# Kernel tuning notes

Measured on AMD Instinct MI355X. Metric: run time of the kernel, lower is better.

Reference implementation:

```python
import jax, jax.numpy as jnp
import numpy as np

N_NODES = 100000
N_EDGES = 1600000
N_FEAT = 128
N_HID = 128
N_CLASS = 10
N_GRAPHS = 512
BN_EPS = 1e-5


def setup_inputs() -> dict:
    key = jax.random.key(0)
    ks = jax.random.split(key, 12)
    x = jax.random.normal(ks[0], (N_NODES, N_FEAT), dtype=jnp.float32)
    edge_index = jax.random.randint(ks[1], (2, N_EDGES), 0, N_NODES, dtype=jnp.int32)
    batch = jnp.sort(jax.random.randint(ks[2], (N_NODES,), 0, N_GRAPHS, dtype=jnp.int32))
    s1 = 1.0 / np.sqrt(N_FEAT)
    s2 = 1.0 / np.sqrt(N_HID)
    W1 = jax.random.uniform(ks[3], (N_FEAT, N_HID), jnp.float32, -s1, s1)
    b1 = jax.random.uniform(ks[4], (N_HID,), jnp.float32, -s1, s1)
    gamma = jnp.ones((N_HID,), jnp.float32)
    beta = jnp.zeros((N_HID,), jnp.float32)
    W2 = jax.random.uniform(ks[5], (N_HID, N_HID), jnp.float32, -s2, s2)
    b2 = jax.random.uniform(ks[6], (N_HID,), jnp.float32, -s2, s2)
    clsW = jax.random.uniform(ks[7], (N_HID, N_CLASS), jnp.float32, -s2, s2)
    clsb = jax.random.uniform(ks[8], (N_CLASS,), jnp.float32, -s2, s2)
    return {"x": x, "edge_index": edge_index, "batch": batch,
            "W1": W1, "b1": b1, "gamma": gamma, "beta": beta,
            "W2": W2, "b2": b2, "clsW": clsW, "clsb": clsb}


def _gcn_norm(edge_index, n_nodes):
    # add self-loops, compute symmetric normalization D^-1/2 A_hat D^-1/2
    loops = jnp.arange(n_nodes, dtype=edge_index.dtype)
    src = jnp.concatenate([edge_index[0], loops])
    dst = jnp.concatenate([edge_index[1], loops])
    deg = jax.ops.segment_sum(jnp.ones_like(dst, dtype=jnp.float32), dst,
                              num_segments=n_nodes)
    dinv = jnp.where(deg > 0, jax.lax.rsqrt(deg), 0.0)
    norm = dinv[src] * dinv[dst]  # [E + N]
    return src, dst, norm


def _gcn_conv(h, src, dst, norm, W, b, n_nodes):
    h = h @ W                                   # [N, nhid] dense GEMM
    msg = h[src] * norm[:, None]                # gather + scale  [E+N, nhid]
    out = jax.ops.segment_sum(msg, dst, num_segments=n_nodes)  # scatter-add
    return out + b


def reference(x, edge_index, batch, W1, b1, gamma, beta, W2, b2, clsW, clsb):
    n_nodes = x.shape[0]
    src, dst, norm = _gcn_norm(edge_index, n_nodes)
    # layer 1: GCNConv -> BatchNorm(eval, running stats 0/1) -> ReLU -> Dropout(eval=id)
    h = _gcn_conv(x, src, dst, norm, W1, b1, n_nodes)
    h = h * (gamma / jnp.sqrt(1.0 + BN_EPS)) + beta
    h = jax.nn.relu(h)
    # layer 2: GCNConv (output layer, no bn/act)
    h = _gcn_conv(h, src, dst, norm, W2, b2, n_nodes)
    # global mean pool over batch index
    sums = jax.ops.segment_sum(h, batch, num_segments=N_GRAPHS)          # [G, nhid]
    cnts = jax.ops.segment_sum(jnp.ones((n_nodes,), h.dtype), batch,
                               num_segments=N_GRAPHS)
    g = sums / jnp.maximum(cnts, 1.0)[:, None]
    out = jax.nn.log_softmax(g @ clsW + clsb, axis=1)                    # [G, nclass]
    return out, g
```

## Files before the change

### kernel.cpp

```cpp
#include <hip/hip_runtime.h>
#include <hip/hip_bf16.h>

#define N_NODES 100000
#define N_EDGES 1600000
#define N_FEAT 128
#define N_HID 128
#define N_CLASS 10
#define N_GRAPHS 512
#define BN_RSQRT 0.9999950000374997f

#define NRANGE 12500
#define NSUB 512
#define SCAP 640
#define HGROUP 64
#define BPB (NSUB / HGROUP)

typedef _Float16 half_t;
typedef __attribute__((ext_vector_type(2))) _Float16 half2v;
typedef __attribute__((ext_vector_type(4))) _Float16 half4v;
typedef __attribute__((ext_vector_type(8))) _Float16 half8v;
typedef __attribute__((ext_vector_type(4))) float floatx4;
typedef __attribute__((ext_vector_type(2))) float floatx2;

__global__ __launch_bounds__(256) void bucket_fused(
    const int* __restrict__ src, const int* __restrict__ dst,
    int* __restrict__ cnt, unsigned long long* __restrict__ bucketed,
    const float* __restrict__ W1, half_t* __restrict__ Wt1,
    const float* __restrict__ W2, half_t* __restrict__ Wt2,
    const int* __restrict__ batch, int* __restrict__ boffs,
    int chunkE, int E, int nnodes)
{
    __shared__ int wcnt[4][8];
    __shared__ int wbase[4][8];
    int blk = blockIdx.x;
    if (blk >= NSUB) {
        int k = blk - NSUB;
        if (k < 128) {
            int i = k * 256 + threadIdx.x;
            const float* W = (i < 16384) ? W1 : W2;
            half_t* Wt = (i < 16384) ? Wt1 : Wt2;
            int j = i & 16383;
            int c = j >> 7, kk = j & 127;
            Wt[(size_t)c * 128 + kk] = (half_t)W[(size_t)kk * 128 + c];
        } else {
            int i = (k - 128) * 256 + threadIdx.x;
            if (i < nnodes) {
                int b = batch[i];
                int prev = (i == 0) ? -1 : batch[i - 1];
                for (int g = prev + 1; g <= b; ++g) boffs[g] = i;
                if (i == nnodes - 1)
                    for (int g = b + 1; g <= N_GRAPHS; ++g) boffs[g] = nnodes;
            }
        }
        return;
    }
    int b = blk;
    int wave = threadIdx.x >> 6;
    int lane = threadIdx.x & 63;
    int e0 = b * chunkE;
    int e1 = e0 + chunkE < E ? e0 + chunkE : E;
    int iters = (chunkE + 255) / 256;

    int mycnt = 0;
    for (int it = 0; it < iters; ++it) {
        int e = e0 + it * 256 + threadIdx.x;
        bool valid = e < e1;
        int d = valid ? dst[e] : 0;
        int rr = (d * 8) / N_NODES;
#pragma unroll
        for (int r = 0; r < 8; ++r) {
            unsigned long long m = __ballot(valid && rr == r);
            if (lane == r) mycnt += __popcll(m);
        }
    }
    if (lane < 8) wcnt[wave][lane] = mycnt;
    __syncthreads();
    if (threadIdx.x < 8) {
        int r = threadIdx.x;
        int s = 0;
#pragma unroll
        for (int w = 0; w < 4; ++w) { wbase[w][r] = s; s += wcnt[w][r]; }
        cnt[r * NSUB + b] = s;
    }
    __syncthreads();

    int myoff = (lane < 8) ? wbase[wave][lane] : 0;
    for (int it = 0; it < iters; ++it) {
        int e = e0 + it * 256 + threadIdx.x;
        bool valid = e < e1;
        int s = valid ? src[e] : 0;
        int d = valid ? dst[e] : 0;
        int rr = (d * 8) / N_NODES;
        unsigned long long pk = ((unsigned long long)(unsigned)d << 32) | (unsigned)s;
#pragma unroll
        for (int r = 0; r < 8; ++r) {
            unsigned long long m = __ballot(valid && rr == r);
            int base_r = __shfl(myoff, r);
            if (valid && rr == r) {
                int pos = base_r + __popcll(m & ((1ull << lane) - 1));
                if (pos < SCAP)
                    bucketed[(size_t)(r * NSUB + b) * SCAP + pos] = pk;
            }
            if (lane == r) myoff += __popcll(m);
        }
    }
}

__global__ __launch_bounds__(256) void hist2(
    const unsigned long long* __restrict__ bucketed, const int* __restrict__ cnt,
    int* __restrict__ partial)
{
    __shared__ int h[NRANGE];
    int r = blockIdx.x & 7, g = blockIdx.x >> 3;
    for (int i = threadIdx.x; i < NRANGE; i += 256) h[i] = 0;
    __syncthreads();
    int rbase = r * NRANGE;
    for (int j = 0; j < BPB; ++j) {
        int b = g * BPB + j;
        int n = cnt[r * NSUB + b];
        if (n > SCAP) n = SCAP;
        const unsigned long long* seg = bucketed + (size_t)(r * NSUB + b) * SCAP;
        for (int i = threadIdx.x; i < n; i += 256)
            atomicAdd(&h[(int)(seg[i] >> 32) - rbase], 1);
    }
    __syncthreads();
    int* slice = partial + (size_t)(r * HGROUP + g) * NRANGE;
    for (int i = threadIdx.x; i < NRANGE; i += 256) slice[i] = h[i];
}

__global__ void deg_reduce(const int* __restrict__ partial, int* __restrict__ deg,
                           float* __restrict__ dinv, int* __restrict__ bsums, int n) {
    __shared__ int sm[256];
    int t = threadIdx.x;
    int i = blockIdx.x * 256 + t;
    int s = 0;
    if (i < n) {
        int rr = i / NRANGE;
        int dl = i - rr * NRANGE;
        const int* p = partial + (size_t)rr * HGROUP * NRANGE + dl;
#pragma unroll 8
        for (int g = 0; g < HGROUP; ++g) s += p[(size_t)g * NRANGE];
        deg[i] = s;
        dinv[i] = rsqrtf((float)s + 1.0f);
    }
    sm[t] = s;
    __syncthreads();
    for (int off = 128; off > 0; off >>= 1) {
        if (t < off) sm[t] += sm[t + off];
        __syncthreads();
    }
    if (t == 0) bsums[blockIdx.x] = sm[0];
}

__global__ void scan_small(int* __restrict__ bsums, int nb) {
    __shared__ int buf[1024];
    int t = threadIdx.x;
    int v = (t < nb) ? bsums[t] : 0;
    buf[t] = v;
    __syncthreads();
    for (int off = 1; off < 1024; off <<= 1) {
        int x = (t >= off) ? buf[t - off] : 0;
        __syncthreads();
        buf[t] += x;
        __syncthreads();
    }
    if (t < nb) bsums[t] = buf[t] - v;
}

__global__ void scan_final_chunkoff(const int* __restrict__ in, const int* __restrict__ bsums,
                                    int* __restrict__ rowptr, int* __restrict__ partial,
                                    int n, int total) {
    __shared__ int s[256];
    int t = threadIdx.x;
    int i = blockIdx.x * 256 + t;
    int v = (i < n) ? in[i] : 0;
    s[t] = v;
    __syncthreads();
    for (int off = 1; off < 256; off <<= 1) {
        int x = (t >= off) ? s[t - off] : 0;
        __syncthreads();
        s[t] += x;
        __syncthreads();
    }
    if (i == 0) rowptr[n] = total;
    if (i < n) {
        int excl = bsums[blockIdx.x] + s[t] - v;
        rowptr[i] = excl;
        int rr = i / NRANGE;
        int dl = i - rr * NRANGE;
        int* p = partial + (size_t)rr * HGROUP * NRANGE + dl;
        int running = excl;
        for (int g = 0; g < HGROUP; ++g) {
            int tmp = p[(size_t)g * NRANGE];
            p[(size_t)g * NRANGE] = running;
            running += tmp;
        }
    }
}

__global__ __launch_bounds__(256) void fill2(
    const unsigned long long* __restrict__ bucketed, const int* __restrict__ cnt,
    const int* __restrict__ partial, int* __restrict__ col)
{
    __shared__ int off[NRANGE];
    int r = blockIdx.x & 7, g = blockIdx.x >> 3;
    const int* slice = partial + (size_t)(r * HGROUP + g) * NRANGE;
    for (int i = threadIdx.x; i < NRANGE; i += 256) off[i] = slice[i];
    __syncthreads();
    int rbase = r * NRANGE;
    for (int j = 0; j < BPB; ++j) {
        int b = g * BPB + j;
        int n = cnt[r * NSUB + b];
        if (n > SCAP) n = SCAP;
        const unsigned long long* seg = bucketed + (size_t)(r * NSUB + b) * SCAP;
        for (int i = threadIdx.x; i < n; i += 256) {
            unsigned long long pk = seg[i];
            int pos = atomicAdd(&off[(int)(pk >> 32) - rbase], 1);
            col[pos] = (int)((unsigned)(pk & 0xffffffffu) << 7);
        }
    }
}

__global__ __launch_bounds__(256) void gemm1_mfma(
    const float* __restrict__ X, const half_t* __restrict__ Wt,
    const float* __restrict__ dinv, unsigned char* __restrict__ Y8, int nrows)
{
    int wave = threadIdx.x >> 6;
    int lane = threadIdx.x & 63;
    int n16  = lane & 15;
    int quad = lane >> 4;
    int r0 = blockIdx.x * 64 + wave * 16;
    if (r0 >= nrows) return;
    int row = r0 + n16;
    const float4* xrow = (const float4*)(X + (size_t)row * 128);
    half8v a[4];
#pragma unroll
    for (int kc = 0; kc < 4; ++kc) {
        float4 f0 = xrow[kc * 8 + quad * 2];
        float4 f1 = xrow[kc * 8 + quad * 2 + 1];
        half8v t = {(half_t)f0.x, (half_t)f0.y, (half_t)f0.z, (half_t)f0.w,
                    (half_t)f1.x, (half_t)f1.y, (half_t)f1.z, (half_t)f1.w};
        a[kc] = t;
    }
    float dr = dinv[row];
#pragma unroll
    for (int c = 0; c < 8; ++c) {
        const half8v* wrow = (const half8v*)(Wt + (size_t)(c * 16 + n16) * 128);
        floatx4 acc = {0.f, 0.f, 0.f, 0.f};
        acc = __builtin_amdgcn_mfma_f32_16x16x32_f16(wrow[0 * 4 + quad], a[0], acc, 0, 0, 0);
        acc = __builtin_amdgcn_mfma_f32_16x16x32_f16(wrow[1 * 4 + quad], a[1], acc, 0, 0, 0);
        acc = __builtin_amdgcn_mfma_f32_16x16x32_f16(wrow[2 * 4 + quad], a[2], acc, 0, 0, 0);
        acc = __builtin_amdgcn_mfma_f32_16x16x32_f16(wrow[3 * 4 + quad], a[3], acc, 0, 0, 0);
        int packed = __builtin_amdgcn_cvt_pk_fp8_f32(acc[0] * dr, acc[1] * dr, 0, false);
        packed = __builtin_amdgcn_cvt_pk_fp8_f32(acc[2] * dr, acc[3] * dr, packed, true);
        *(int*)(Y8 + (size_t)row * 128 + c * 16 + quad * 4) = packed;
    }
}

__global__ __launch_bounds__(256) void gemm2_mfma(
    const half_t* __restrict__ X, const half_t* __restrict__ Wt,
    const float* __restrict__ dinv, unsigned char* __restrict__ Y8, int nrows)
{
    int wave = threadIdx.x >> 6;
    int lane = threadIdx.x & 63;
    int n16  = lane & 15;
    int quad = lane >> 4;
    int r0 = blockIdx.x * 64 + wave * 16;
    if (r0 >= nrows) return;
    int row = r0 + n16;
    const half8v* xrow = (const half8v*)(X + (size_t)row * 128);
    half8v a0 = xrow[0 * 4 + quad];
    half8v a1 = xrow[1 * 4 + quad];
    half8v a2 = xrow[2 * 4 + quad];
    half8v a3 = xrow[3 * 4 + quad];
    float dr = dinv[row];
#pragma unroll
    for (int c = 0; c < 8; ++c) {
        const half8v* wrow = (const half8v*)(Wt + (size_t)(c * 16 + n16) * 128);
        floatx4 acc = {0.f, 0.f, 0.f, 0.f};
        acc = __builtin_amdgcn_mfma_f32_16x16x32_f16(wrow[0 * 4 + quad], a0, acc, 0, 0, 0);
        acc = __builtin_amdgcn_mfma_f32_16x16x32_f16(wrow[1 * 4 + quad], a1, acc, 0, 0, 0);
        acc = __builtin_amdgcn_mfma_f32_16x16x32_f16(wrow[2 * 4 + quad], a2, acc, 0, 0, 0);
        acc = __builtin_amdgcn_mfma_f32_16x16x32_f16(wrow[3 * 4 + quad], a3, acc, 0, 0, 0);
        int packed = __builtin_amdgcn_cvt_pk_fp8_f32(acc[0] * dr, acc[1] * dr, 0, false);
        packed = __builtin_amdgcn_cvt_pk_fp8_f32(acc[2] * dr, acc[3] * dr, packed, true);
        *(int*)(Y8 + (size_t)row * 128 + c * 16 + quad * 4) = packed;
    }
}

__global__ __launch_bounds__(256) void agg_fp8(
    const unsigned char* __restrict__ hs, half_t* __restrict__ out,
    const int* __restrict__ col, const int* __restrict__ rowptr,
    const float* __restrict__ dinv, const float* __restrict__ bias,
    const float* __restrict__ gamma, const float* __restrict__ beta,
    int nnodes, int do_bn_relu)
{
    int wave = threadIdx.x >> 6;
    int lane = threadIdx.x & 63;
    int i = blockIdx.x * 4 + wave;
    if (i >= nnodes) return;
    int hf = lane >> 5;
    unsigned f4 = (unsigned)(lane & 31) << 2;
    unsigned ZOFF = (unsigned)nnodes << 7;
    int e0 = rowptr[i], e1 = rowptr[i + 1];
    floatx2 a01 = {0.f, 0.f}, a23 = {0.f, 0.f};
    floatx2 b01 = {0.f, 0.f}, b23 = {0.f, 0.f};
    for (int base = e0; base < e1; base += 64) {
        int idx = base + lane;
        unsigned ecol = (idx < e1) ? (unsigned)col[idx] : ZOFF;
        int lim = base + 64 < e1 ? base + 64 : e1;
        for (int e = base; e < lim; e += 16) {
            int j = e - base + hf;
            unsigned s0 = __shfl(ecol, j + 0);
            unsigned s1 = __shfl(ecol, j + 2);
            unsigned s2 = __shfl(ecol, j + 4);
            unsigned s3 = __shfl(ecol, j + 6);
            unsigned s4 = __shfl(ecol, j + 8);
            unsigned s5 = __shfl(ecol, j + 10);
            unsigned s6 = __shfl(ecol, j + 12);
            unsigned s7 = __shfl(ecol, j + 14);
            unsigned v0 = *(const unsigned*)(hs + (s0 | f4));
            unsigned v1 = *(const unsigned*)(hs + (s1 | f4));
            unsigned v2 = *(const unsigned*)(hs + (s2 | f4));
            unsigned v3 = *(const unsigned*)(hs + (s3 | f4));
            unsigned v4 = *(const unsigned*)(hs + (s4 | f4));
            unsigned v5 = *(const unsigned*)(hs + (s5 | f4));
            unsigned v6 = *(const unsigned*)(hs + (s6 | f4));
            unsigned v7 = *(const unsigned*)(hs + (s7 | f4));
            a01 += __builtin_amdgcn_cvt_pk_f32_fp8((int)v0, false);
            a23 += __builtin_amdgcn_cvt_pk_f32_fp8((int)v0, true);
            b01 += __builtin_amdgcn_cvt_pk_f32_fp8((int)v1, false);
            b23 += __builtin_amdgcn_cvt_pk_f32_fp8((int)v1, true);
            a01 += __builtin_amdgcn_cvt_pk_f32_fp8((int)v2, false);
            a23 += __builtin_amdgcn_cvt_pk_f32_fp8((int)v2, true);
            b01 += __builtin_amdgcn_cvt_pk_f32_fp8((int)v3, false);
            b23 += __builtin_amdgcn_cvt_pk_f32_fp8((int)v3, true);
            a01 += __builtin_amdgcn_cvt_pk_f32_fp8((int)v4, false);
            a23 += __builtin_amdgcn_cvt_pk_f32_fp8((int)v4, true);
            b01 += __builtin_amdgcn_cvt_pk_f32_fp8((int)v5, false);
            b23 += __builtin_amdgcn_cvt_pk_f32_fp8((int)v5, true);
            a01 += __builtin_amdgcn_cvt_pk_f32_fp8((int)v6, false);
            a23 += __builtin_amdgcn_cvt_pk_f32_fp8((int)v6, true);
            b01 += __builtin_amdgcn_cvt_pk_f32_fp8((int)v7, false);
            b23 += __builtin_amdgcn_cvt_pk_f32_fp8((int)v7, true);
        }
    }
    a01 += b01;
    a23 += b23;
    float c0 = a01.x + __shfl_xor(a01.x, 32);
    float c1 = a01.y + __shfl_xor(a01.y, 32);
    float c2 = a23.x + __shfl_xor(a23.x, 32);
    float c3 = a23.y + __shfl_xor(a23.y, 32);
    if (hf == 0) {
        unsigned vs = *(const unsigned*)(hs + (((unsigned)i << 7) | f4));
        floatx2 fs01 = __builtin_amdgcn_cvt_pk_f32_fp8((int)vs, false);
        floatx2 fs23 = __builtin_amdgcn_cvt_pk_f32_fp8((int)vs, true);
        float di = dinv[i];
        float4 bi = *(const float4*)(bias + f4);
        float o0 = di * (c0 + fs01.x) + bi.x;
        float o1 = di * (c1 + fs01.y) + bi.y;
        float o2 = di * (c2 + fs23.x) + bi.z;
        float o3 = di * (c3 + fs23.y) + bi.w;
        if (do_bn_relu) {
            float4 ga = *(const float4*)(gamma + f4);
            float4 be = *(const float4*)(beta + f4);
            o0 = fmaf(o0, ga.x * BN_RSQRT, be.x);
            o1 = fmaf(o1, ga.y * BN_RSQRT, be.y);
            o2 = fmaf(o2, ga.z * BN_RSQRT, be.z);
            o3 = fmaf(o3, ga.w * BN_RSQRT, be.w);
            o0 = o0 > 0.f ? o0 : 0.f;
            o1 = o1 > 0.f ? o1 : 0.f;
            o2 = o2 > 0.f ? o2 : 0.f;
            o3 = o3 > 0.f ? o3 : 0.f;
        }
        half4v ov = {(half_t)o0, (half_t)o1, (half_t)o2, (half_t)o3};
        *(half4v*)(out + (size_t)i * 128 + f4) = ov;
    }
}

__global__ __launch_bounds__(512) void pool_cls(
    const half_t* __restrict__ h, const int* __restrict__ boffs,
    const float* __restrict__ clsW, const float* __restrict__ clsb,
    float* __restrict__ gout, float* __restrict__ out)
{
    __shared__ float red[8][128];
    __shared__ float zbuf[16];
    int g = blockIdx.x;
    int w = threadIdx.x >> 6;
    int lane = threadIdx.x & 63;
    int n0 = boffs[g], n1 = boffs[g + 1];
    float ax = 0.f, ay = 0.f;
    for (int n = n0 + w; n < n1; n += 8) {
        half2v v = *(const half2v*)(h + (size_t)n * 128 + lane * 2);
        ax += (float)v.x;
        ay += (float)v.y;
    }
    red[w][lane * 2] = ax;
    red[w][lane * 2 + 1] = ay;
    __syncthreads();
    if (w == 0) {
        float sx = 0.f, sy = 0.f;
#pragma unroll
        for (int j = 0; j < 8; ++j) {
            sx += red[j][lane * 2];
            sy += red[j][lane * 2 + 1];
        }
        float cnt = (float)((n1 - n0) > 1 ? (n1 - n0) : 1);
        float g0 = sx / cnt, g1 = sy / cnt;
        gout[(size_t)g * 128 + lane * 2] = g0;
        gout[(size_t)g * 128 + lane * 2 + 1] = g1;
        red[0][lane * 2] = g0;
        red[0][lane * 2 + 1] = g1;
    }
    __syncthreads();
    if (threadIdx.x < N_CLASS) {
        int c = threadIdx.x;
        float z = clsb[c];
        for (int k = 0; k < N_HID; ++k)
            z = fmaf(red[0][k], clsW[k * N_CLASS + c], z);
        zbuf[c] = z;
    }
    __syncthreads();
    if (threadIdx.x == 0) {
        float m = zbuf[0];
#pragma unroll
        for (int c = 1; c < N_CLASS; ++c) m = fmaxf(m, zbuf[c]);
        float s = 0.f;
#pragma unroll
        for (int c = 0; c < N_CLASS; ++c) s += expf(zbuf[c] - m);
        float l = logf(s);
#pragma unroll
        for (int c = 0; c < N_CLASS; ++c)
            out[(size_t)g * N_CLASS + c] = zbuf[c] - m - l;
    }
}

extern "C" void kernel_launch(void* const* d_in, const int* in_sizes, int n_in,
                              void* d_out, int out_size, void* d_ws, size_t ws_size,
                              hipStream_t stream) {
    const float* x     = (const float*)d_in[0];
    const int*   ei    = (const int*)d_in[1];
    const int*   batch = (const int*)d_in[2];
    const float* W1    = (const float*)d_in[3];
    const float* b1    = (const float*)d_in[4];
    const float* gamma = (const float*)d_in[5];
    const float* beta  = (const float*)d_in[6];
    const float* W2    = (const float*)d_in[7];
    const float* b2    = (const float*)d_in[8];
    const float* clsW  = (const float*)d_in[9];
    const float* clsb  = (const float*)d_in[10];

    const int N = in_sizes[0] / N_FEAT;
    const int E = in_sizes[1] / 2;
    const int* src = ei;
    const int* dst = ei + E;

    unsigned char* BA8 = (unsigned char*)d_ws;
    half_t* BB = (half_t*)(BA8 + (size_t)(N + 1) * 128);
    half_t* Wt1 = BB + (size_t)N * 128;
    half_t* Wt2 = Wt1 + 16384;
    int*   col     = (int*)(Wt2 + 16384);
    int*   rowptr  = col + E;
    int*   deg     = rowptr + (N + 4);
    float* dinv    = (float*)(deg + N);
    int*   cnt     = (int*)(dinv + N);
    unsigned long long* bucketed =
        (unsigned long long*)(cnt + 8 * NSUB);
    int*   partial = (int*)(bucketed + (size_t)8 * NSUB * SCAP);
    int*   boffs   = partial + 8 * HGROUP * NRANGE;
    int*   bsums   = boffs + N_GRAPHS + 4;

    const int nb = (N + 255) / 256;
    const int chunkE = (E + NSUB - 1) / NSUB;
    const int gemmBlocks = (N + 63) / 64;

    hipMemsetAsync(BA8 + (size_t)N * 128, 0, 128, stream);

    bucket_fused<<<NSUB + 128 + nb, 256, 0, stream>>>(
        src, dst, cnt, bucketed, W1, Wt1, W2, Wt2, batch, boffs, chunkE, E, N);
    hist2<<<8 * HGROUP, 256, 0, stream>>>(bucketed, cnt, partial);
    deg_reduce<<<nb, 256, 0, stream>>>(partial, deg, dinv, bsums, N);
    scan_small<<<1, 1024, 0, stream>>>(bsums, nb);
    scan_final_chunkoff<<<nb, 256, 0, stream>>>(deg, bsums, rowptr, partial, N, E);
    gemm1_mfma<<<gemmBlocks, 256, 0, stream>>>(x, Wt1, dinv, BA8, N);
    fill2<<<8 * HGROUP, 256, 0, stream>>>(bucketed, cnt, partial, col);
    agg_fp8<<<(N + 3) / 4, 256, 0, stream>>>(BA8, BB, col, rowptr, dinv, b1, gamma, beta, N, 1);
    gemm2_mfma<<<gemmBlocks, 256, 0, stream>>>(BB, Wt2, dinv, BA8, N);
    agg_fp8<<<(N + 3) / 4, 256, 0, stream>>>(BA8, BB, col, rowptr, dinv, b2, gamma, beta, N, 0);

    float* out = (float*)d_out;
    float* gsec = out + (size_t)N_GRAPHS * N_CLASS;
    pool_cls<<<N_GRAPHS, 512, 0, stream>>>(BB, boffs, clsW, clsb, gsec, out);
}
```

Before: 336.5 us.

## Bucket edges per wave in a single pass and widen agg loads to 8 bytes

The bucketing kernel now gives each wave its own segment, so the separate counting pass and the block-level syncs are gone and the dst array is read only once. Segment capacity shrinks and hist2/fill2 walk four times as many smaller segments. The aggregation kernel now has 16 lanes cover a row with 8-byte fp8 loads and processes four edges per step, with a two-stage shuffle reduction and a 16-byte fp16 store. The smaller per-wave capacity (192 against an expected ~100 edges per range) raises overflow risk if the edge distribution is skewed.

```diff
diff --git a/kernel.cpp b/kernel.cpp
--- a/kernel.cpp
+++ b/kernel.cpp
@@ -11,14 +11,15 @@
 
 #define NRANGE 12500
 #define NSUB 512
-#define SCAP 640
+#define NSEG (NSUB * 4)
+#define SCAP 192
 #define HGROUP 64
-#define BPB (NSUB / HGROUP)
+#define CPB (NSEG / HGROUP)
 
 typedef _Float16 half_t;
 typedef __attribute__((ext_vector_type(2))) _Float16 half2v;
-typedef __attribute__((ext_vector_type(4))) _Float16 half4v;
 typedef __attribute__((ext_vector_type(8))) _Float16 half8v;
+typedef __attribute__((ext_vector_type(8))) _Float16 half8v2;
 typedef __attribute__((ext_vector_type(4))) float floatx4;
 typedef __attribute__((ext_vector_type(2))) float floatx2;
 
@@ -30,8 +31,6 @@
     const int* __restrict__ batch, int* __restrict__ boffs,
     int chunkE, int E, int nnodes)
 {
-    __shared__ int wcnt[4][8];
-    __shared__ int wbase[4][8];
     int blk = blockIdx.x;
     if (blk >= NSUB) {
         int k = blk - NSUB;
@@ -57,36 +56,13 @@
     int b = blk;
     int wave = threadIdx.x >> 6;
     int lane = threadIdx.x & 63;
+    int cell = b * 4 + wave;
     int e0 = b * chunkE;
     int e1 = e0 + chunkE < E ? e0 + chunkE : E;
     int iters = (chunkE + 255) / 256;
-
-    int mycnt = 0;
+    int myoff = 0;
     for (int it = 0; it < iters; ++it) {
-        int e = e0 + it * 256 + threadIdx.x;
-        bool valid = e < e1;
-        int d = valid ? dst[e] : 0;
-        int rr = (d * 8) / N_NODES;
-#pragma unroll
-        for (int r = 0; r < 8; ++r) {
-            unsigned long long m = __ballot(valid && rr == r);
-            if (lane == r) mycnt += __popcll(m);
-        }
-    }
-    if (lane < 8) wcnt[wave][lane] = mycnt;
-    __syncthreads();
-    if (threadIdx.x < 8) {
-        int r = threadIdx.x;
-        int s = 0;
-#pragma unroll
-        for (int w = 0; w < 4; ++w) { wbase[w][r] = s; s += wcnt[w][r]; }
-        cnt[r * NSUB + b] = s;
-    }
-    __syncthreads();
-
-    int myoff = (lane < 8) ? wbase[wave][lane] : 0;
-    for (int it = 0; it < iters; ++it) {
-        int e = e0 + it * 256 + threadIdx.x;
+        int e = e0 + it * 256 + wave * 64 + lane;
         bool valid = e < e1;
         int s = valid ? src[e] : 0;
         int d = valid ? dst[e] : 0;
@@ -99,11 +75,12 @@
             if (valid && rr == r) {
                 int pos = base_r + __popcll(m & ((1ull << lane) - 1));
                 if (pos < SCAP)
-                    bucketed[(size_t)(r * NSUB + b) * SCAP + pos] = pk;
+                    bucketed[(size_t)(r * NSEG + cell) * SCAP + pos] = pk;
             }
             if (lane == r) myoff += __popcll(m);
         }
     }
+    if (lane < 8) cnt[lane * NSEG + cell] = myoff;
 }
 
 __global__ __launch_bounds__(256) void hist2(
@@ -115,11 +92,11 @@
     for (int i = threadIdx.x; i < NRANGE; i += 256) h[i] = 0;
     __syncthreads();
     int rbase = r * NRANGE;
-    for (int j = 0; j < BPB; ++j) {
-        int b = g * BPB + j;
-        int n = cnt[r * NSUB + b];
+    for (int j = 0; j < CPB; ++j) {
+        int c = g * CPB + j;
+        int n = cnt[r * NSEG + c];
         if (n > SCAP) n = SCAP;
-        const unsigned long long* seg = bucketed + (size_t)(r * NSUB + b) * SCAP;
+        const unsigned long long* seg = bucketed + (size_t)(r * NSEG + c) * SCAP;
         for (int i = threadIdx.x; i < n; i += 256)
             atomicAdd(&h[(int)(seg[i] >> 32) - rbase], 1);
     }
@@ -208,11 +185,11 @@
     for (int i = threadIdx.x; i < NRANGE; i += 256) off[i] = slice[i];
     __syncthreads();
     int rbase = r * NRANGE;
-    for (int j = 0; j < BPB; ++j) {
-        int b = g * BPB + j;
-        int n = cnt[r * NSUB + b];
+    for (int j = 0; j < CPB; ++j) {
+        int c = g * CPB + j;
+        int n = cnt[r * NSEG + c];
         if (n > SCAP) n = SCAP;
-        const unsigned long long* seg = bucketed + (size_t)(r * NSUB + b) * SCAP;
+        const unsigned long long* seg = bucketed + (size_t)(r * NSEG + c) * SCAP;
         for (int i = threadIdx.x; i < n; i += 256) {
             unsigned long long pk = seg[i];
             int pos = atomicAdd(&off[(int)(pk >> 32) - rbase], 1);
@@ -299,82 +276,82 @@
     int lane = threadIdx.x & 63;
     int i = blockIdx.x * 4 + wave;
     if (i >= nnodes) return;
-    int hf = lane >> 5;
-    unsigned f4 = (unsigned)(lane & 31) << 2;
+    int q = lane >> 4;
+    unsigned f8 = (unsigned)(lane & 15) << 3;
     unsigned ZOFF = (unsigned)nnodes << 7;
     int e0 = rowptr[i], e1 = rowptr[i + 1];
-    floatx2 a01 = {0.f, 0.f}, a23 = {0.f, 0.f};
-    floatx2 b01 = {0.f, 0.f}, b23 = {0.f, 0.f};
+    floatx2 a01 = {0.f, 0.f}, a23 = {0.f, 0.f}, a45 = {0.f, 0.f}, a67 = {0.f, 0.f};
+    floatx2 c01 = {0.f, 0.f}, c23 = {0.f, 0.f}, c45 = {0.f, 0.f}, c67 = {0.f, 0.f};
     for (int base = e0; base < e1; base += 64) {
         int idx = base + lane;
         unsigned ecol = (idx < e1) ? (unsigned)col[idx] : ZOFF;
         int lim = base + 64 < e1 ? base + 64 : e1;
         for (int e = base; e < lim; e += 16) {
-            int j = e - base + hf;
+            int j = e - base + q;
             unsigned s0 = __shfl(ecol, j + 0);
-            unsigned s1 = __shfl(ecol, j + 2);
-            unsigned s2 = __shfl(ecol, j + 4);
-            unsigned s3 = __shfl(ecol, j + 6);
-            unsigned s4 = __shfl(ecol, j + 8);
-            unsigned s5 = __shfl(ecol, j + 10);
-            unsigned s6 = __shfl(ecol, j + 12);
-            unsigned s7 = __shfl(ecol, j + 14);
-            unsigned v0 = *(const unsigned*)(hs + (s0 | f4));
-            unsigned v1 = *(const unsigned*)(hs + (s1 | f4));
-            unsigned v2 = *(const unsigned*)(hs + (s2 | f4));
-            unsigned v3 = *(const unsigned*)(hs + (s3 | f4));
-            unsigned v4 = *(const unsigned*)(hs + (s4 | f4));
-            unsigned v5 = *(const unsigned*)(hs + (s5 | f4));
-            unsigned v6 = *(const unsigned*)(hs + (s6 | f4));
-            unsigned v7 = *(const unsigned*)(hs + (s7 | f4));
-            a01 += __builtin_amdgcn_cvt_pk_f32_fp8((int)v0, false);
-            a23 += __builtin_amdgcn_cvt_pk_f32_fp8((int)v0, true);
-            b01 += __builtin_amdgcn_cvt_pk_f32_fp8((int)v1, false);
-            b23 += __builtin_amdgcn_cvt_pk_f32_fp8((int)v1, true);
-            a01 += __builtin_amdgcn_cvt_pk_f32_fp8((int)v2, false);
-            a23 += __builtin_amdgcn_cvt_pk_f32_fp8((int)v2, true);
-            b01 += __builtin_amdgcn_cvt_pk_f32_fp8((int)v3, false);
-            b23 += __builtin_amdgcn_cvt_pk_f32_fp8((int)v3, true);
-            a01 += __builtin_amdgcn_cvt_pk_f32_fp8((int)v4, false);
-            a23 += __builtin_amdgcn_cvt_pk_f32_fp8((int)v4, true);
-            b01 += __builtin_amdgcn_cvt_pk_f32_fp8((int)v5, false);
-            b23 += __builtin_amdgcn_cvt_pk_f32_fp8((int)v5, true);
-            a01 += __builtin_amdgcn_cvt_pk_f32_fp8((int)v6, false);
-            a23 += __builtin_amdgcn_cvt_pk_f32_fp8((int)v6, true);
-            b01 += __builtin_amdgcn_cvt_pk_f32_fp8((int)v7, false);
-            b23 += __builtin_amdgcn_cvt_pk_f32_fp8((int)v7, true);
-        }
-    }
-    a01 += b01;
-    a23 += b23;
-    float c0 = a01.x + __shfl_xor(a01.x, 32);
-    float c1 = a01.y + __shfl_xor(a01.y, 32);
-    float c2 = a23.x + __shfl_xor(a23.x, 32);
-    float c3 = a23.y + __shfl_xor(a23.y, 32);
-    if (hf == 0) {
-        unsigned vs = *(const unsigned*)(hs + (((unsigned)i << 7) | f4));
-        floatx2 fs01 = __builtin_amdgcn_cvt_pk_f32_fp8((int)vs, false);
-        floatx2 fs23 = __builtin_amdgcn_cvt_pk_f32_fp8((int)vs, true);
+            unsigned s1 = __shfl(ecol, j + 4);
+            unsigned s2 = __shfl(ecol, j + 8);
+            unsigned s3 = __shfl(ecol, j + 12);
+            uint2 v0 = *(const uint2*)(hs + (s0 | f8));
+            uint2 v1 = *(const uint2*)(hs + (s1 | f8));
+            uint2 v2 = *(const uint2*)(hs + (s2 | f8));
+            uint2 v3 = *(const uint2*)(hs + (s3 | f8));
+            a01 += __builtin_amdgcn_cvt_pk_f32_fp8((int)v0.x, false);
+            a23 += __builtin_amdgcn_cvt_pk_f32_fp8((int)v0.x, true);
+            a45 += __builtin_amdgcn_cvt_pk_f32_fp8((int)v0.y, false);
+            a67 += __builtin_amdgcn_cvt_pk_f32_fp8((int)v0.y, true);
+            c01 += __builtin_amdgcn_cvt_pk_f32_fp8((int)v1.x, false);
+            c23 += __builtin_amdgcn_cvt_pk_f32_fp8((int)v1.x, true);
+            c45 += __builtin_amdgcn_cvt_pk_f32_fp8((int)v1.y, false);
+            c67 += __builtin_amdgcn_cvt_pk_f32_fp8((int)v1.y, true);
+            a01 += __builtin_amdgcn_cvt_pk_f32_fp8((int)v2.x, false);
+            a23 += __builtin_amdgcn_cvt_pk_f32_fp8((int)v2.x, true);
+            a45 += __builtin_amdgcn_cvt_pk_f32_fp8((int)v2.y, false);
+            a67 += __builtin_amdgcn_cvt_pk_f32_fp8((int)v2.y, true);
+            c01 += __builtin_amdgcn_cvt_pk_f32_fp8((int)v3.x, false);
+            c23 += __builtin_amdgcn_cvt_pk_f32_fp8((int)v3.x, true);
+            c45 += __builtin_amdgcn_cvt_pk_f32_fp8((int)v3.y, false);
+            c67 += __builtin_amdgcn_cvt_pk_f32_fp8((int)v3.y, true);
+        }
+    }
+    a01 += c01; a23 += c23; a45 += c45; a67 += c67;
+    float f[8] = {a01.x, a01.y, a23.x, a23.y, a45.x, a45.y, a67.x, a67.y};
+#pragma unroll
+    for (int k = 0; k < 8; ++k) {
+        f[k] += __shfl_xor(f[k], 16);
+        f[k] += __shfl_xor(f[k], 32);
+    }
+    if (q == 0) {
+        int w = lane & 15;
+        uint2 vs = *(const uint2*)(hs + (((unsigned)i << 7) | f8));
+        floatx2 s01 = __builtin_amdgcn_cvt_pk_f32_fp8((int)vs.x, false);
+        floatx2 s23 = __builtin_amdgcn_cvt_pk_f32_fp8((int)vs.x, true);
+        floatx2 s45 = __builtin_amdgcn_cvt_pk_f32_fp8((int)vs.y, false);
+        floatx2 s67 = __builtin_amdgcn_cvt_pk_f32_fp8((int)vs.y, true);
+        float sf[8] = {s01.x, s01.y, s23.x, s23.y, s45.x, s45.y, s67.x, s67.y};
         float di = dinv[i];
-        float4 bi = *(const float4*)(bias + f4);
-        float o0 = di * (c0 + fs01.x) + bi.x;
-        float o1 = di * (c1 + fs01.y) + bi.y;
-        float o2 = di * (c2 + fs23.x) + bi.z;
-        float o3 = di * (c3 + fs23.y) + bi.w;
+        float o[8];
+        float4 bi0 = *(const float4*)(bias + w * 8);
+        float4 bi1 = *(const float4*)(bias + w * 8 + 4);
+        float bb[8] = {bi0.x, bi0.y, bi0.z, bi0.w, bi1.x, bi1.y, bi1.z, bi1.w};
+#pragma unroll
+        for (int k = 0; k < 8; ++k) o[k] = di * (f[k] + sf[k]) + bb[k];
         if (do_bn_relu) {
-            float4 ga = *(const float4*)(gamma + f4);
-            float4 be = *(const float4*)(beta + f4);
-            o0 = fmaf(o0, ga.x * BN_RSQRT, be.x);
-            o1 = fmaf(o1, ga.y * BN_RSQRT, be.y);
-            o2 = fmaf(o2, ga.z * BN_RSQRT, be.z);
-            o3 = fmaf(o3, ga.w * BN_RSQRT, be.w);
-            o0 = o0 > 0.f ? o0 : 0.f;
-            o1 = o1 > 0.f ? o1 : 0.f;
-            o2 = o2 > 0.f ? o2 : 0.f;
-            o3 = o3 > 0.f ? o3 : 0.f;
-        }
-        half4v ov = {(half_t)o0, (half_t)o1, (half_t)o2, (half_t)o3};
-        *(half4v*)(out + (size_t)i * 128 + f4) = ov;
+            float4 ga0 = *(const float4*)(gamma + w * 8);
+            float4 ga1 = *(const float4*)(gamma + w * 8 + 4);
+            float4 be0 = *(const float4*)(beta + w * 8);
+            float4 be1 = *(const float4*)(beta + w * 8 + 4);
+            float gg[8] = {ga0.x, ga0.y, ga0.z, ga0.w, ga1.x, ga1.y, ga1.z, ga1.w};
+            float ee[8] = {be0.x, be0.y, be0.z, be0.w, be1.x, be1.y, be1.z, be1.w};
+#pragma unroll
+            for (int k = 0; k < 8; ++k) {
+                o[k] = fmaf(o[k], gg[k] * BN_RSQRT, ee[k]);
+                o[k] = o[k] > 0.f ? o[k] : 0.f;
+            }
+        }
+        half8v ov = {(half_t)o[0], (half_t)o[1], (half_t)o[2], (half_t)o[3],
+                     (half_t)o[4], (half_t)o[5], (half_t)o[6], (half_t)o[7]};
+        *(half8v*)(out + (size_t)i * 128 + w * 8) = ov;
     }
 }
 
@@ -465,8 +442,8 @@
     float* dinv    = (float*)(deg + N);
     int*   cnt     = (int*)(dinv + N);
     unsigned long long* bucketed =
-        (unsigned long long*)(cnt + 8 * NSUB);
-    int*   partial = (int*)(bucketed + (size_t)8 * NSUB * SCAP);
+        (unsigned long long*)(cnt + 8 * NSEG);
+    int*   partial = (int*)(bucketed + (size_t)8 * NSEG * SCAP);
     int*   boffs   = partial + 8 * HGROUP * NRANGE;
     int*   bsums   = boffs + N_GRAPHS + 4;
 
```

Result: slower. 348.2 us (+3.5%).
